# Kernel optimization log

Hardware: AMD Instinct MI355X
Metric: run time of the kernel (lower is better)

The kernel has to match this reference:

```python
import jax, jax.numpy as jnp
import numpy as np

B, T, I, H = 4096, 512, 4, 64  # batch, seq_len, input_size, hidden_size


def setup_inputs() -> dict:
    key = jax.random.key(0)
    ks = jax.random.split(key, 13)
    sc = 1.0 / np.sqrt(H)
    sc2 = 1.0 / np.sqrt(32)
    n = lambda k, shape, s: (jax.random.normal(k, shape, jnp.float32) * s)
    return {
        "x": jax.random.normal(ks[0], (B, T, I), jnp.float32),
        # PyTorch LSTM layout: gates stacked as [i, f, g, o] along first dim
        "w_ih0": n(ks[1], (4 * H, I), sc),
        "w_hh0": n(ks[2], (4 * H, H), sc),
        "b_ih0": n(ks[3], (4 * H,), sc),
        "b_hh0": n(ks[4], (4 * H,), sc),
        "w_ih1": n(ks[5], (4 * H, H), sc),
        "w_hh1": n(ks[6], (4 * H, H), sc),
        "b_ih1": n(ks[7], (4 * H,), sc),
        "b_hh1": n(ks[8], (4 * H,), sc),
        "fc1_w": n(ks[9], (32, H), sc),
        "fc1_b": n(ks[10], (32,), sc),
        "fc2_w": n(ks[11], (2, 32), sc2),
        "fc2_b": n(ks[12], (2,), sc2),
    }


def _lstm_layer(x, w_ih, w_hh, b_ih, b_hh):
    # x: [B, T, D_in] -> hidden sequence [B, T, H]
    Bq = x.shape[0]
    Hq = w_hh.shape[1]
    # Precompute input contribution for all timesteps in one GEMM
    pre = jnp.einsum('bti,gi->btg', x, w_ih) + b_ih + b_hh  # [B, T, 4H]
    pre = jnp.swapaxes(pre, 0, 1)  # [T, B, 4H] for scan

    def step(carry, xt):
        h, c = carry
        gates = xt + h @ w_hh.T  # [B, 4H]
        i, f, g, o = jnp.split(gates, 4, axis=-1)
        c_new = jax.nn.sigmoid(f) * c + jax.nn.sigmoid(i) * jnp.tanh(g)
        h_new = jax.nn.sigmoid(o) * jnp.tanh(c_new)
        return (h_new, c_new), h_new

    h0 = jnp.zeros((Bq, Hq), x.dtype)
    _, hs = jax.lax.scan(step, (h0, h0), pre)
    return jnp.swapaxes(hs, 0, 1)  # [B, T, H]


def reference(x, w_ih0, w_hh0, b_ih0, b_hh0, w_ih1, w_hh1, b_ih1, b_hh1,
              fc1_w, fc1_b, fc2_w, fc2_b):
    h1 = _lstm_layer(x, w_ih0, w_hh0, b_ih0, b_hh0)
    # dropout(p=0.2) between LSTM layers is inactive in eval mode
    h2 = _lstm_layer(h1, w_ih1, w_hh1, b_ih1, b_hh1)
    last = h2[:, -1, :]  # [B, H]
    y = jax.nn.relu(last @ fc1_w.T + fc1_b)
    return jax.nn.relu(y @ fc2_w.T + fc2_b)  # [B, 2]
```

## Files before the change

### kernel.cpp

```cpp
#include <hip/hip_runtime.h>

#define TT 512
#define MM 16

typedef _Float16 f16_t;
typedef f16_t f16x8 __attribute__((ext_vector_type(8)));
typedef float  f32x4 __attribute__((ext_vector_type(4)));
typedef unsigned uintx4 __attribute__((ext_vector_type(4)));

#define MFMA16(A, B, C) __builtin_amdgcn_mfma_f32_16x16x32_f16((A), (B), (C), 0, 0, 0)

__device__ __forceinline__ float fr(float x) { return __builtin_amdgcn_rcpf(x); }

#if __has_builtin(__builtin_amdgcn_exp2f)
__device__ __forceinline__ float ex2(float x) { return __builtin_amdgcn_exp2f(x); }
#define EXS 1.44269504f
#else
__device__ __forceinline__ float ex2(float x) { return __expf(x); }
#define EXS 1.0f
#endif

#if __has_builtin(__builtin_amdgcn_cvt_pkrtz)
__device__ __forceinline__ unsigned pk2(float a, float b) {
    auto p = __builtin_amdgcn_cvt_pkrtz(a, b);
    return __builtin_bit_cast(unsigned, p);
}
#else
__device__ __forceinline__ unsigned pk2(float a, float b) {
    unsigned short ha = __builtin_bit_cast(unsigned short, (f16_t)a);
    unsigned short hb = __builtin_bit_cast(unsigned short, (f16_t)b);
    return (unsigned)ha | ((unsigned)hb << 16);
}
#endif

__device__ __forceinline__ void bar() {
    asm volatile("s_waitcnt lgkmcnt(0)" ::: "memory");
    __builtin_amdgcn_s_barrier();
    asm volatile("" ::: "memory");
}

__device__ __forceinline__ float cellEW(float pi, float pf, float pg, float po,
                                        float4 bq, float& c) {
    float A = ex2(fmaf(pf, -EXS, bq.y));
    float B = ex2(fmaf(pi, -EXS, bq.x));
    float C = ex2(fmaf(pg, 2.f * EXS, bq.z));
    float oa = 1.f + A;
    float u  = (1.f + B) * (C + 1.f);
    float cn = fmaf(c, u, oa * (C - 1.f)) * fr(oa * u);
    c = cn;
    float D = ex2(fmaf(po, -EXS, bq.w));
    float E = ex2(fminf(2.f * EXS * cn, 30.f));
    return (E - 1.f) * fr((1.f + D) * (E + 1.f));
}

__device__ __forceinline__ f16x8 cvt8(const float* p) {
    f16x8 r;
#pragma unroll
    for (int e = 0; e < 8; ++e) r[e] = (f16_t)p[e];
    return r;
}


__global__ __launch_bounds__(512, 2) void lstm_v11(
    const float* __restrict__ x,
    const float* __restrict__ w_ih0, const float* __restrict__ w_hh0,
    const float* __restrict__ b_ih0, const float* __restrict__ b_hh0,
    const float* __restrict__ w_ih1, const float* __restrict__ w_hh1,
    const float* __restrict__ b_ih1, const float* __restrict__ b_hh1,
    const float* __restrict__ fc1_w, const float* __restrict__ fc1_b,
    const float* __restrict__ fc2_w, const float* __restrict__ fc2_b,
    float* __restrict__ out)
{
    __shared__ __align__(16) unsigned h1p[2][512];
    __shared__ __align__(16) unsigned h2p[2][512];
    __shared__ __align__(16) float sH[MM * 68];
    __shared__ float sY[MM * 34];

    const int tid = threadIdx.x;
    const int l   = tid & 63;
    const int wv  = tid >> 6;
    const int rbase = blockIdx.x * MM;

    const int lc = l & 15;
    const int lq = l >> 4;
    const bool isL1 = (wv >= 4);
    const int wsub = wv & 3;
    const int hc0  = wsub * 16 + lq * 4;
    const int swz  = (lc & 7) << 4;

    const int rdo0 = (lc * 128 + 0 * 64 + lq * 16) ^ swz;
    const int rdo1 = (lc * 128 + 1 * 64 + lq * 16) ^ swz;
    const int wro  = (lc * 128 + hc0 * 2) ^ swz;
    const unsigned xmask = (lq == 0) ? 0xFFFFFFFFu : 0u;

    f16x8 wA[4][2];
    f16x8 wB[4][2];
    f16x8 wx[4];
    float4 bq[4];
#pragma unroll
    for (int g = 0; g < 4; ++g) {
        const int grow = (g * 64 + wsub * 16 + lc) * 64 + lq * 8;
        if (isL1) {
            wA[g][0] = cvt8(w_hh0 + grow);
            wA[g][1] = cvt8(w_hh0 + grow + 32);
            const int ga = (g * 64 + wsub * 16 + lc) * 4;
#pragma unroll
            for (int e = 0; e < 8; ++e)
                wx[g][e] = (e < 4 && lq == 0) ? (f16_t)w_ih0[ga + e] : (f16_t)0.f;
        } else {
            wA[g][0] = cvt8(w_ih1 + grow);
            wA[g][1] = cvt8(w_ih1 + grow + 32);
            wB[g][0] = cvt8(w_hh1 + grow);
            wB[g][1] = cvt8(w_hh1 + grow + 32);
        }
    }
#pragma unroll
    for (int q = 0; q < 4; ++q) {
        const int hc = hc0 + q;
        float b[4];
#pragma unroll
        for (int g = 0; g < 4; ++g) {
            const int ga = g * 64 + hc;
            b[g] = isL1 ? (b_ih0[ga] + b_hh0[ga]) : (b_ih1[ga] + b_hh1[ga]);
        }
        bq[q] = make_float4(-EXS * b[0], -EXS * b[1], 2.f * EXS * b[2], -EXS * b[3]);
    }

    float c_st[4] = {0.f, 0.f, 0.f, 0.f};
    const f32x4 z4 = {0.f, 0.f, 0.f, 0.f};

    const float4* xg = (const float4*)x;
    const size_t xrow = (size_t)(rbase + lc) * TT;
    float4 xq = make_float4(0, 0, 0, 0);
    const float4* xp = xg + xrow + 2;
    if (isL1) xq = xg[xrow + 1];

    if (isL1) {
        float4 x0 = xg[xrow + 0];
        unsigned a0 = pk2(x0.x, x0.y) & xmask, a1 = pk2(x0.z, x0.w) & xmask;
        uintx4 uv = {a0, a1, 0u, 0u};
        f16x8 xf = __builtin_bit_cast(f16x8, uv);
        f32x4 a[4];
#pragma unroll
        for (int g = 0; g < 4; ++g) a[g] = MFMA16(wx[g], xf, z4);
        float hv[4];
#pragma unroll
        for (int q = 0; q < 4; ++q)
            hv[q] = cellEW(a[0][q], a[1][q], a[2][q], a[3][q], bq[q], c_st[q]);
        uint2 w2 = make_uint2(pk2(hv[0], hv[1]), pk2(hv[2], hv[3]));
        *(uint2*)((char*)h1p[0] + wro) = w2;
    } else {
        h2p[0][tid] = 0;
        h2p[0][256 + tid] = 0;
    }
    __syncthreads();

    auto STEP = [&](const unsigned* h1r, unsigned* h1w,
                    const unsigned* h2r, unsigned* h2w,
                    bool l1act, bool pref, bool lastStore) {
        if (isL1) {
            if (l1act) {
                const char* pl = (const char*)h1r;
                f16x8 hf0 = *(const f16x8*)(pl + rdo0);
                f16x8 hf1 = *(const f16x8*)(pl + rdo1);
                float4 xn;
                if (pref) { xn = *xp; ++xp; }
                unsigned a0 = pk2(xq.x, xq.y) & xmask, a1 = pk2(xq.z, xq.w) & xmask;
                uintx4 uv = {a0, a1, 0u, 0u};
                f16x8 xf = __builtin_bit_cast(f16x8, uv);

                f32x4 a[4];
                __builtin_amdgcn_s_setprio(1);
#pragma unroll
                for (int g = 0; g < 4; ++g) {
                    a[g] = MFMA16(wx[g], xf, z4);
                    a[g] = MFMA16(wA[g][0], hf0, a[g]);
                    a[g] = MFMA16(wA[g][1], hf1, a[g]);
                }
                __builtin_amdgcn_s_setprio(0);

                float hv[4];
#pragma unroll
                for (int q = 0; q < 4; ++q)
                    hv[q] = cellEW(a[0][q], a[1][q], a[2][q], a[3][q], bq[q], c_st[q]);
                uint2 w2 = make_uint2(pk2(hv[0], hv[1]), pk2(hv[2], hv[3]));
                *(uint2*)((char*)h1w + wro) = w2;
                if (pref) xq = xn;
            }
        } else {
            const char* pl1 = (const char*)h1r;
            const char* pl2 = (const char*)h2r;
            f16x8 hf0 = *(const f16x8*)(pl1 + rdo0);
            f16x8 hf1 = *(const f16x8*)(pl1 + rdo1);
            f16x8 gf0 = *(const f16x8*)(pl2 + rdo0);
            f16x8 gf1 = *(const f16x8*)(pl2 + rdo1);

            f32x4 a[4];
            __builtin_amdgcn_s_setprio(1);
#pragma unroll
            for (int g = 0; g < 4; ++g) {
                a[g] = MFMA16(wA[g][0], hf0, z4);
                a[g] = MFMA16(wA[g][1], hf1, a[g]);
                a[g] = MFMA16(wB[g][0], gf0, a[g]);
                a[g] = MFMA16(wB[g][1], gf1, a[g]);
            }
            __builtin_amdgcn_s_setprio(0);

            float hv[4];
#pragma unroll
            for (int q = 0; q < 4; ++q)
                hv[q] = cellEW(a[0][q], a[1][q], a[2][q], a[3][q], bq[q], c_st[q]);
            uint2 w2 = make_uint2(pk2(hv[0], hv[1]), pk2(hv[2], hv[3]));
            *(uint2*)((char*)h2w + wro) = w2;
            if (lastStore)
                *(float4*)&sH[lc * 68 + hc0] = make_float4(hv[0], hv[1], hv[2], hv[3]);
        }
        bar();
    };

    for (int it = 0; it < 255; ++it) {
        STEP(h1p[0], h1p[1], h2p[0], h2p[1], true, true, false);
        STEP(h1p[1], h1p[0], h2p[1], h2p[0], true, true, false);
    }
    STEP(h1p[0], h1p[1], h2p[0], h2p[1], true, false, false);
    STEP(h1p[1], h1p[0], h2p[1], h2p[0], false, false, true);

    {
        const int r = tid >> 5, mo = tid & 31;
        float s = fc1_b[mo];
#pragma unroll 8
        for (int k = 0; k < 64; ++k) s = fmaf(sH[r * 68 + k], fc1_w[mo * 64 + k], s);
        sY[r * 34 + mo] = fmaxf(s, 0.f);
    }
    __syncthreads();
    if (tid < 32) {
        const int r = tid >> 1, o = tid & 1;
        float s = fc2_b[o];
#pragma unroll 8
        for (int mo = 0; mo < 32; ++mo) s = fmaf(sY[r * 34 + mo], fc2_w[o * 32 + mo], s);
        out[(size_t)(rbase + r) * 2 + o] = fmaxf(s, 0.f);
    }
}

extern "C" void kernel_launch(void* const* d_in, const int* in_sizes, int n_in,
                              void* d_out, int out_size, void* d_ws, size_t ws_size,
                              hipStream_t stream) {
    const float* x     = (const float*)d_in[0];
    const float* w_ih0 = (const float*)d_in[1];
    const float* w_hh0 = (const float*)d_in[2];
    const float* b_ih0 = (const float*)d_in[3];
    const float* b_hh0 = (const float*)d_in[4];
    const float* w_ih1 = (const float*)d_in[5];
    const float* w_hh1 = (const float*)d_in[6];
    const float* b_ih1 = (const float*)d_in[7];
    const float* b_hh1 = (const float*)d_in[8];
    const float* fc1_w = (const float*)d_in[9];
    const float* fc1_b = (const float*)d_in[10];
    const float* fc2_w = (const float*)d_in[11];
    const float* fc2_b = (const float*)d_in[12];
    float* out = (float*)d_out;

    const int nB   = in_sizes[0] / (TT * 4);
    const int grid = nB / MM;

    lstm_v11<<<grid, 512, 0, stream>>>(x, w_ih0, w_hh0, b_ih0, b_hh0,
                                       w_ih1, w_hh1, b_ih1, b_hh1,
                                       fc1_w, fc1_b, fc2_w, fc2_b, out);
}
```

Measured before the change: 370.2 us.

## Split each LSTM step into two phases so MFMA and elementwise overlap across layers

Each timestep now runs in two barrier-separated phases. Layer-1 waves do their MFMAs while layer-2 waves do the elementwise cell update for the previous step, and then the roles swap. Layer-2 gate accumulators are carried across phases in registers, and its hidden state drops to a single shared buffer. The goal is to keep the matrix unit and vector ALU busy at the same time instead of running each wave's MFMA and transcendental work back to back. In exchange there are twice as many block barriers per timestep and extra live registers, which could hurt occupancy at 512 threads with 2 blocks.

```diff
diff --git a/kernel.cpp b/kernel.cpp
--- a/kernel.cpp
+++ b/kernel.cpp
@@ -61,7 +61,7 @@
 }
 
 
-__global__ __launch_bounds__(512, 2) void lstm_v11(
+__global__ __launch_bounds__(512, 2) void lstm_v12(
     const float* __restrict__ x,
     const float* __restrict__ w_ih0, const float* __restrict__ w_hh0,
     const float* __restrict__ b_ih0, const float* __restrict__ b_hh0,
@@ -72,7 +72,7 @@
     float* __restrict__ out)
 {
     __shared__ __align__(16) unsigned h1p[2][512];
-    __shared__ __align__(16) unsigned h2p[2][512];
+    __shared__ __align__(16) unsigned h2p[512];
     __shared__ __align__(16) float sH[MM * 68];
     __shared__ float sY[MM * 34];
 
@@ -128,6 +128,7 @@
 
     float c_st[4] = {0.f, 0.f, 0.f, 0.f};
     const f32x4 z4 = {0.f, 0.f, 0.f, 0.f};
+    f32x4 a2s[4];
 
     const float4* xg = (const float4*)x;
     const size_t xrow = (size_t)(rbase + lc) * TT;
@@ -137,8 +138,8 @@
 
     if (isL1) {
         float4 x0 = xg[xrow + 0];
-        unsigned a0 = pk2(x0.x, x0.y) & xmask, a1 = pk2(x0.z, x0.w) & xmask;
-        uintx4 uv = {a0, a1, 0u, 0u};
+        unsigned u0 = pk2(x0.x, x0.y) & xmask, u1 = pk2(x0.z, x0.w) & xmask;
+        uintx4 uv = {u0, u1, 0u, 0u};
         f16x8 xf = __builtin_bit_cast(f16x8, uv);
         f32x4 a[4];
 #pragma unroll
@@ -150,14 +151,14 @@
         uint2 w2 = make_uint2(pk2(hv[0], hv[1]), pk2(hv[2], hv[3]));
         *(uint2*)((char*)h1p[0] + wro) = w2;
     } else {
-        h2p[0][tid] = 0;
-        h2p[0][256 + tid] = 0;
+        h2p[tid] = 0;
+        h2p[256 + tid] = 0;
     }
     __syncthreads();
 
     auto STEP = [&](const unsigned* h1r, unsigned* h1w,
-                    const unsigned* h2r, unsigned* h2w,
-                    bool l1act, bool pref, bool lastStore) {
+                    bool l1act, bool pref, bool ew2act) {
+        f32x4 a1[4];
         if (isL1) {
             if (l1act) {
                 const char* pl = (const char*)h1r;
@@ -165,65 +166,76 @@
                 f16x8 hf1 = *(const f16x8*)(pl + rdo1);
                 float4 xn;
                 if (pref) { xn = *xp; ++xp; }
-                unsigned a0 = pk2(xq.x, xq.y) & xmask, a1 = pk2(xq.z, xq.w) & xmask;
-                uintx4 uv = {a0, a1, 0u, 0u};
+                unsigned u0 = pk2(xq.x, xq.y) & xmask, u1 = pk2(xq.z, xq.w) & xmask;
+                uintx4 uv = {u0, u1, 0u, 0u};
                 f16x8 xf = __builtin_bit_cast(f16x8, uv);
-
-                f32x4 a[4];
                 __builtin_amdgcn_s_setprio(1);
 #pragma unroll
                 for (int g = 0; g < 4; ++g) {
-                    a[g] = MFMA16(wx[g], xf, z4);
-                    a[g] = MFMA16(wA[g][0], hf0, a[g]);
-                    a[g] = MFMA16(wA[g][1], hf1, a[g]);
+                    a1[g] = MFMA16(wx[g], xf, z4);
+                    a1[g] = MFMA16(wA[g][0], hf0, a1[g]);
+                    a1[g] = MFMA16(wA[g][1], hf1, a1[g]);
                 }
                 __builtin_amdgcn_s_setprio(0);
-
+                if (pref) xq = xn;
+            }
+        } else {
+            if (ew2act) {
                 float hv[4];
 #pragma unroll
                 for (int q = 0; q < 4; ++q)
-                    hv[q] = cellEW(a[0][q], a[1][q], a[2][q], a[3][q], bq[q], c_st[q]);
+                    hv[q] = cellEW(a2s[0][q], a2s[1][q], a2s[2][q], a2s[3][q], bq[q], c_st[q]);
+                uint2 w2 = make_uint2(pk2(hv[0], hv[1]), pk2(hv[2], hv[3]));
+                *(uint2*)((char*)h2p + wro) = w2;
+            }
+        }
+        bar();
+        if (isL1) {
+            if (l1act) {
+                float hv[4];
+#pragma unroll
+                for (int q = 0; q < 4; ++q)
+                    hv[q] = cellEW(a1[0][q], a1[1][q], a1[2][q], a1[3][q], bq[q], c_st[q]);
                 uint2 w2 = make_uint2(pk2(hv[0], hv[1]), pk2(hv[2], hv[3]));
                 *(uint2*)((char*)h1w + wro) = w2;
-                if (pref) xq = xn;
             }
         } else {
             const char* pl1 = (const char*)h1r;
-            const char* pl2 = (const char*)h2r;
+            const char* pl2 = (const char*)h2p;
             f16x8 hf0 = *(const f16x8*)(pl1 + rdo0);
             f16x8 hf1 = *(const f16x8*)(pl1 + rdo1);
             f16x8 gf0 = *(const f16x8*)(pl2 + rdo0);
             f16x8 gf1 = *(const f16x8*)(pl2 + rdo1);
-
-            f32x4 a[4];
             __builtin_amdgcn_s_setprio(1);
 #pragma unroll
             for (int g = 0; g < 4; ++g) {
-                a[g] = MFMA16(wA[g][0], hf0, z4);
-                a[g] = MFMA16(wA[g][1], hf1, a[g]);
-                a[g] = MFMA16(wB[g][0], gf0, a[g]);
-                a[g] = MFMA16(wB[g][1], gf1, a[g]);
+                a2s[g] = MFMA16(wA[g][0], hf0, z4);
+                a2s[g] = MFMA16(wA[g][1], hf1, a2s[g]);
+                a2s[g] = MFMA16(wB[g][0], gf0, a2s[g]);
+                a2s[g] = MFMA16(wB[g][1], gf1, a2s[g]);
             }
             __builtin_amdgcn_s_setprio(0);
-
-            float hv[4];
-#pragma unroll
-            for (int q = 0; q < 4; ++q)
-                hv[q] = cellEW(a[0][q], a[1][q], a[2][q], a[3][q], bq[q], c_st[q]);
-            uint2 w2 = make_uint2(pk2(hv[0], hv[1]), pk2(hv[2], hv[3]));
-            *(uint2*)((char*)h2w + wro) = w2;
-            if (lastStore)
-                *(float4*)&sH[lc * 68 + hc0] = make_float4(hv[0], hv[1], hv[2], hv[3]);
         }
         bar();
     };
 
-    for (int it = 0; it < 255; ++it) {
-        STEP(h1p[0], h1p[1], h2p[0], h2p[1], true, true, false);
-        STEP(h1p[1], h1p[0], h2p[1], h2p[0], true, true, false);
-    }
-    STEP(h1p[0], h1p[1], h2p[0], h2p[1], true, false, false);
-    STEP(h1p[1], h1p[0], h2p[1], h2p[0], false, false, true);
+    STEP(h1p[0], h1p[1], true, true, false);
+    for (int k = 0; k < 254; ++k) {
+        STEP(h1p[1], h1p[0], true, true, true);
+        STEP(h1p[0], h1p[1], true, true, true);
+    }
+    STEP(h1p[1], h1p[0], true, true,  true);
+    STEP(h1p[0], h1p[1], true, false, true);
+    STEP(h1p[1], h1p[0], false, false, true);
+
+    if (!isL1) {
+        float hv[4];
+#pragma unroll
+        for (int q = 0; q < 4; ++q)
+            hv[q] = cellEW(a2s[0][q], a2s[1][q], a2s[2][q], a2s[3][q], bq[q], c_st[q]);
+        *(float4*)&sH[lc * 68 + hc0] = make_float4(hv[0], hv[1], hv[2], hv[3]);
+    }
+    __syncthreads();
 
     {
         const int r = tid >> 5, mo = tid & 31;
@@ -263,7 +275,7 @@
     const int nB   = in_sizes[0] / (TT * 4);
     const int grid = nB / MM;
 
-    lstm_v11<<<grid, 512, 0, stream>>>(x, w_ih0, w_hh0, b_ih0, b_hh0,
+    lstm_v12<<<grid, 512, 0, stream>>>(x, w_ih0, w_hh0, b_ih0, b_hh0,
                                        w_ih1, w_hh1, b_ih1, b_hh1,
                                        fc1_w, fc1_b, fc2_w, fc2_b, out);
 }
```

Measured after the change: 436.1 us. 1.18x slower.

## Stage packed fp16 input sequence in LDS up front; raise layer-2 wave priority

Applied to the files above, without the earlier changes.

Before the recurrence, the block loads the full 16-row x 512-step input tile, packs it to fp16 and stores it in 64KB of dynamic shared memory. Each layer-1 step then reads its x fragment from LDS instead of issuing a global load on the serial critical path. Lanes that previously masked x to zero now read from a small zero buffer. The per-step setprio toggles are replaced by a persistent high priority for the layer-2 waves. LDS use rises to about 80KB per block, which at two blocks per CU may limit occupancy, and there is an upfront load phase before any compute starts.

```diff
diff --git a/kernel.cpp b/kernel.cpp
--- a/kernel.cpp
+++ b/kernel.cpp
@@ -61,7 +61,9 @@
 }
 
 
-__global__ __launch_bounds__(512, 2) void lstm_v11(
+#define SMEM_BYTES 80272
+
+__global__ __launch_bounds__(512, 2) void lstm_v14(
     const float* __restrict__ x,
     const float* __restrict__ w_ih0, const float* __restrict__ w_hh0,
     const float* __restrict__ b_ih0, const float* __restrict__ b_hh0,
@@ -71,10 +73,13 @@
     const float* __restrict__ fc2_w, const float* __restrict__ fc2_b,
     float* __restrict__ out)
 {
-    __shared__ __align__(16) unsigned h1p[2][512];
-    __shared__ __align__(16) unsigned h2p[2][512];
-    __shared__ __align__(16) float sH[MM * 68];
-    __shared__ float sY[MM * 34];
+    extern __shared__ __align__(16) char sm[];
+    unsigned* xpk = (unsigned*)(sm);
+    unsigned (*h1p)[512] = (unsigned(*)[512])(sm + 65536);
+    unsigned (*h2p)[512] = (unsigned(*)[512])(sm + 69632);
+    unsigned* zq = (unsigned*)(sm + 73728);
+    float* sH = (float*)(sm + 73744);
+    float* sY = (float*)(sm + 78096);
 
     const int tid = threadIdx.x;
     const int l   = tid & 63;
@@ -91,7 +96,21 @@
     const int rdo0 = (lc * 128 + 0 * 64 + lq * 16) ^ swz;
     const int rdo1 = (lc * 128 + 1 * 64 + lq * 16) ^ swz;
     const int wro  = (lc * 128 + hc0 * 2) ^ swz;
-    const unsigned xmask = (lq == 0) ? 0xFFFFFFFFu : 0u;
+
+    {
+        const float4* xsrc = (const float4*)x;
+        for (int j = tid; j < 16 * 512; j += 512) {
+            const int row = j >> 9;
+            const int tt  = j & 511;
+            float4 v = xsrc[(size_t)(rbase + row) * TT + tt];
+            uint2 w = make_uint2(pk2(v.x, v.y), pk2(v.z, v.w));
+            *(uint2*)((char*)xpk + (size_t)(tt * 16 + row) * 8) = w;
+        }
+        if (tid == 0) { zq[0] = 0; zq[1] = 0; zq[2] = 0; zq[3] = 0; }
+    }
+    const char* xbp  = (lq == 0) ? ((const char*)xpk + (16 + lc) * 8) : (const char*)zq;
+    const char* x0p  = (lq == 0) ? ((const char*)xpk + lc * 8)        : (const char*)zq;
+    const int   xstr = (lq == 0) ? 128 : 0;
 
     f16x8 wA[4][2];
     f16x8 wB[4][2];
@@ -129,16 +148,11 @@
     float c_st[4] = {0.f, 0.f, 0.f, 0.f};
     const f32x4 z4 = {0.f, 0.f, 0.f, 0.f};
 
-    const float4* xg = (const float4*)x;
-    const size_t xrow = (size_t)(rbase + lc) * TT;
-    float4 xq = make_float4(0, 0, 0, 0);
-    const float4* xp = xg + xrow + 2;
-    if (isL1) xq = xg[xrow + 1];
+    __syncthreads();
 
     if (isL1) {
-        float4 x0 = xg[xrow + 0];
-        unsigned a0 = pk2(x0.x, x0.y) & xmask, a1 = pk2(x0.z, x0.w) & xmask;
-        uintx4 uv = {a0, a1, 0u, 0u};
+        uint2 x0 = *(const uint2*)x0p;
+        uintx4 uv = {x0.x, x0.y, 0u, 0u};
         f16x8 xf = __builtin_bit_cast(f16x8, uv);
         f32x4 a[4];
 #pragma unroll
@@ -154,6 +168,8 @@
         h2p[0][256 + tid] = 0;
     }
     __syncthreads();
+
+    if (!isL1) __builtin_amdgcn_s_setprio(1);
 
     auto STEP = [&](const unsigned* h1r, unsigned* h1w,
                     const unsigned* h2r, unsigned* h2w,
@@ -163,29 +179,24 @@
                 const char* pl = (const char*)h1r;
                 f16x8 hf0 = *(const f16x8*)(pl + rdo0);
                 f16x8 hf1 = *(const f16x8*)(pl + rdo1);
-                float4 xn;
-                if (pref) { xn = *xp; ++xp; }
-                unsigned a0 = pk2(xq.x, xq.y) & xmask, a1 = pk2(xq.z, xq.w) & xmask;
-                uintx4 uv = {a0, a1, 0u, 0u};
+                uint2 xu = *(const uint2*)xbp;
+                if (pref) xbp += xstr;
+                uintx4 uv = {xu.x, xu.y, 0u, 0u};
                 f16x8 xf = __builtin_bit_cast(f16x8, uv);
 
                 f32x4 a[4];
-                __builtin_amdgcn_s_setprio(1);
 #pragma unroll
                 for (int g = 0; g < 4; ++g) {
                     a[g] = MFMA16(wx[g], xf, z4);
                     a[g] = MFMA16(wA[g][0], hf0, a[g]);
                     a[g] = MFMA16(wA[g][1], hf1, a[g]);
                 }
-                __builtin_amdgcn_s_setprio(0);
-
                 float hv[4];
 #pragma unroll
                 for (int q = 0; q < 4; ++q)
                     hv[q] = cellEW(a[0][q], a[1][q], a[2][q], a[3][q], bq[q], c_st[q]);
                 uint2 w2 = make_uint2(pk2(hv[0], hv[1]), pk2(hv[2], hv[3]));
                 *(uint2*)((char*)h1w + wro) = w2;
-                if (pref) xq = xn;
             }
         } else {
             const char* pl1 = (const char*)h1r;
@@ -196,7 +207,6 @@
             f16x8 gf1 = *(const f16x8*)(pl2 + rdo1);
 
             f32x4 a[4];
-            __builtin_amdgcn_s_setprio(1);
 #pragma unroll
             for (int g = 0; g < 4; ++g) {
                 a[g] = MFMA16(wA[g][0], hf0, z4);
@@ -204,8 +214,6 @@
                 a[g] = MFMA16(wB[g][0], gf0, a[g]);
                 a[g] = MFMA16(wB[g][1], gf1, a[g]);
             }
-            __builtin_amdgcn_s_setprio(0);
-
             float hv[4];
 #pragma unroll
             for (int q = 0; q < 4; ++q)
@@ -224,6 +232,8 @@
     }
     STEP(h1p[0], h1p[1], h2p[0], h2p[1], true, false, false);
     STEP(h1p[1], h1p[0], h2p[1], h2p[0], false, false, true);
+
+    if (!isL1) __builtin_amdgcn_s_setprio(0);
 
     {
         const int r = tid >> 5, mo = tid & 31;
@@ -263,7 +273,10 @@
     const int nB   = in_sizes[0] / (TT * 4);
     const int grid = nB / MM;
 
-    lstm_v11<<<grid, 512, 0, stream>>>(x, w_ih0, w_hh0, b_ih0, b_hh0,
-                                       w_ih1, w_hh1, b_ih1, b_hh1,
-                                       fc1_w, fc1_b, fc2_w, fc2_b, out);
-}
+    hipFuncSetAttribute(reinterpret_cast<const void*>(lstm_v14),
+                        hipFuncAttributeMaxDynamicSharedMemorySize, SMEM_BYTES);
+
+    lstm_v14<<<grid, 512, SMEM_BYTES, stream>>>(x, w_ih0, w_hh0, b_ih0, b_hh0,
+                                                w_ih1, w_hh1, b_ih1, b_hh1,
+                                                fc1_w, fc1_b, fc2_w, fc2_b, out);
+}
```

Result: no change. 371.3 us (+0.3%).

## Merge both LSTM layers into each wave, halving block size to four waves

Applied to the files above, without the earlier changes.

Instead of dedicating four waves to layer 1 and four to layer 2, each of four waves now holds weights for both layers and computes both layer recurrences every step. Layer-2 MFMAs are issued first and layer-1 MFMAs are interleaved with the layer-2 cell nonlinearities to overlap matrix and vector work. This reduces the number of waves participating in each barrier but doubles per-wave register pressure and serial work per step, lowering available wave-level parallelism per CU.

```diff
diff --git a/kernel.cpp b/kernel.cpp
--- a/kernel.cpp
+++ b/kernel.cpp
@@ -61,7 +61,7 @@
 }
 
 
-__global__ __launch_bounds__(512, 2) void lstm_v11(
+__global__ __launch_bounds__(256, 1) void lstm_v15(
     const float* __restrict__ x,
     const float* __restrict__ w_ih0, const float* __restrict__ w_hh0,
     const float* __restrict__ b_ih0, const float* __restrict__ b_hh0,
@@ -83,9 +83,7 @@
 
     const int lc = l & 15;
     const int lq = l >> 4;
-    const bool isL1 = (wv >= 4);
-    const int wsub = wv & 3;
-    const int hc0  = wsub * 16 + lq * 4;
+    const int hc0  = wv * 16 + lq * 4;
     const int swz  = (lc & 7) << 4;
 
     const int rdo0 = (lc * 128 + 0 * 64 + lq * 16) ^ swz;
@@ -93,52 +91,52 @@
     const int wro  = (lc * 128 + hc0 * 2) ^ swz;
     const unsigned xmask = (lq == 0) ? 0xFFFFFFFFu : 0u;
 
-    f16x8 wA[4][2];
-    f16x8 wB[4][2];
+    f16x8 w1A[4][2];
     f16x8 wx[4];
-    float4 bq[4];
+    f16x8 w2A[4][2];
+    f16x8 w2B[4][2];
+    float4 bq1[4], bq2[4];
 #pragma unroll
     for (int g = 0; g < 4; ++g) {
-        const int grow = (g * 64 + wsub * 16 + lc) * 64 + lq * 8;
-        if (isL1) {
-            wA[g][0] = cvt8(w_hh0 + grow);
-            wA[g][1] = cvt8(w_hh0 + grow + 32);
-            const int ga = (g * 64 + wsub * 16 + lc) * 4;
-#pragma unroll
-            for (int e = 0; e < 8; ++e)
-                wx[g][e] = (e < 4 && lq == 0) ? (f16_t)w_ih0[ga + e] : (f16_t)0.f;
-        } else {
-            wA[g][0] = cvt8(w_ih1 + grow);
-            wA[g][1] = cvt8(w_ih1 + grow + 32);
-            wB[g][0] = cvt8(w_hh1 + grow);
-            wB[g][1] = cvt8(w_hh1 + grow + 32);
-        }
+        const int grow = (g * 64 + wv * 16 + lc) * 64 + lq * 8;
+        w1A[g][0] = cvt8(w_hh0 + grow);
+        w1A[g][1] = cvt8(w_hh0 + grow + 32);
+        w2A[g][0] = cvt8(w_ih1 + grow);
+        w2A[g][1] = cvt8(w_ih1 + grow + 32);
+        w2B[g][0] = cvt8(w_hh1 + grow);
+        w2B[g][1] = cvt8(w_hh1 + grow + 32);
+        const int ga = (g * 64 + wv * 16 + lc) * 4;
+#pragma unroll
+        for (int e = 0; e < 8; ++e)
+            wx[g][e] = (e < 4 && lq == 0) ? (f16_t)w_ih0[ga + e] : (f16_t)0.f;
     }
 #pragma unroll
     for (int q = 0; q < 4; ++q) {
         const int hc = hc0 + q;
-        float b[4];
+        float b1[4], b2[4];
 #pragma unroll
         for (int g = 0; g < 4; ++g) {
             const int ga = g * 64 + hc;
-            b[g] = isL1 ? (b_ih0[ga] + b_hh0[ga]) : (b_ih1[ga] + b_hh1[ga]);
+            b1[g] = b_ih0[ga] + b_hh0[ga];
+            b2[g] = b_ih1[ga] + b_hh1[ga];
         }
-        bq[q] = make_float4(-EXS * b[0], -EXS * b[1], 2.f * EXS * b[2], -EXS * b[3]);
-    }
-
-    float c_st[4] = {0.f, 0.f, 0.f, 0.f};
+        bq1[q] = make_float4(-EXS * b1[0], -EXS * b1[1], 2.f * EXS * b1[2], -EXS * b1[3]);
+        bq2[q] = make_float4(-EXS * b2[0], -EXS * b2[1], 2.f * EXS * b2[2], -EXS * b2[3]);
+    }
+
+    float c1[4] = {0.f, 0.f, 0.f, 0.f};
+    float c2[4] = {0.f, 0.f, 0.f, 0.f};
     const f32x4 z4 = {0.f, 0.f, 0.f, 0.f};
 
     const float4* xg = (const float4*)x;
     const size_t xrow = (size_t)(rbase + lc) * TT;
-    float4 xq = make_float4(0, 0, 0, 0);
     const float4* xp = xg + xrow + 2;
-    if (isL1) xq = xg[xrow + 1];
-
-    if (isL1) {
+    float4 xq = xg[xrow + 1];
+
+    {
         float4 x0 = xg[xrow + 0];
-        unsigned a0 = pk2(x0.x, x0.y) & xmask, a1 = pk2(x0.z, x0.w) & xmask;
-        uintx4 uv = {a0, a1, 0u, 0u};
+        unsigned u0 = pk2(x0.x, x0.y) & xmask, u1 = pk2(x0.z, x0.w) & xmask;
+        uintx4 uv = {u0, u1, 0u, 0u};
         f16x8 xf = __builtin_bit_cast(f16x8, uv);
         f32x4 a[4];
 #pragma unroll
@@ -146,10 +144,9 @@
         float hv[4];
 #pragma unroll
         for (int q = 0; q < 4; ++q)
-            hv[q] = cellEW(a[0][q], a[1][q], a[2][q], a[3][q], bq[q], c_st[q]);
+            hv[q] = cellEW(a[0][q], a[1][q], a[2][q], a[3][q], bq1[q], c1[q]);
         uint2 w2 = make_uint2(pk2(hv[0], hv[1]), pk2(hv[2], hv[3]));
         *(uint2*)((char*)h1p[0] + wro) = w2;
-    } else {
         h2p[0][tid] = 0;
         h2p[0][256 + tid] = 0;
     }
@@ -158,63 +155,57 @@
     auto STEP = [&](const unsigned* h1r, unsigned* h1w,
                     const unsigned* h2r, unsigned* h2w,
                     bool l1act, bool pref, bool lastStore) {
-        if (isL1) {
-            if (l1act) {
-                const char* pl = (const char*)h1r;
-                f16x8 hf0 = *(const f16x8*)(pl + rdo0);
-                f16x8 hf1 = *(const f16x8*)(pl + rdo1);
-                float4 xn;
-                if (pref) { xn = *xp; ++xp; }
-                unsigned a0 = pk2(xq.x, xq.y) & xmask, a1 = pk2(xq.z, xq.w) & xmask;
-                uintx4 uv = {a0, a1, 0u, 0u};
-                f16x8 xf = __builtin_bit_cast(f16x8, uv);
-
-                f32x4 a[4];
-                __builtin_amdgcn_s_setprio(1);
-#pragma unroll
-                for (int g = 0; g < 4; ++g) {
-                    a[g] = MFMA16(wx[g], xf, z4);
-                    a[g] = MFMA16(wA[g][0], hf0, a[g]);
-                    a[g] = MFMA16(wA[g][1], hf1, a[g]);
-                }
-                __builtin_amdgcn_s_setprio(0);
-
-                float hv[4];
-#pragma unroll
-                for (int q = 0; q < 4; ++q)
-                    hv[q] = cellEW(a[0][q], a[1][q], a[2][q], a[3][q], bq[q], c_st[q]);
-                uint2 w2 = make_uint2(pk2(hv[0], hv[1]), pk2(hv[2], hv[3]));
-                *(uint2*)((char*)h1w + wro) = w2;
-                if (pref) xq = xn;
+        const char* pl1 = (const char*)h1r;
+        const char* pl2 = (const char*)h2r;
+        f16x8 hf0 = *(const f16x8*)(pl1 + rdo0);
+        f16x8 hf1 = *(const f16x8*)(pl1 + rdo1);
+        f16x8 gf0 = *(const f16x8*)(pl2 + rdo0);
+        f16x8 gf1 = *(const f16x8*)(pl2 + rdo1);
+
+        f32x4 a2[4];
+#pragma unroll
+        for (int g = 0; g < 4; ++g) {
+            a2[g] = MFMA16(w2A[g][0], hf0, z4);
+            a2[g] = MFMA16(w2A[g][1], hf1, a2[g]);
+            a2[g] = MFMA16(w2B[g][0], gf0, a2[g]);
+            a2[g] = MFMA16(w2B[g][1], gf1, a2[g]);
+        }
+
+        float hv2[4];
+        if (l1act) {
+            float4 xn;
+            if (pref) { xn = *xp; ++xp; }
+            unsigned u0 = pk2(xq.x, xq.y) & xmask, u1 = pk2(xq.z, xq.w) & xmask;
+            uintx4 uv = {u0, u1, 0u, 0u};
+            f16x8 xf = __builtin_bit_cast(f16x8, uv);
+
+            f32x4 a1[4];
+#pragma unroll
+            for (int j = 0; j < 4; ++j) {
+                a1[j] = MFMA16(wx[j], xf, z4);
+                a1[j] = MFMA16(w1A[j][0], hf0, a1[j]);
+                a1[j] = MFMA16(w1A[j][1], hf1, a1[j]);
+                hv2[j] = cellEW(a2[0][j], a2[1][j], a2[2][j], a2[3][j], bq2[j], c2[j]);
             }
+            uint2 wh2 = make_uint2(pk2(hv2[0], hv2[1]), pk2(hv2[2], hv2[3]));
+            *(uint2*)((char*)h2w + wro) = wh2;
+
+            float hv1[4];
+#pragma unroll
+            for (int q = 0; q < 4; ++q)
+                hv1[q] = cellEW(a1[0][q], a1[1][q], a1[2][q], a1[3][q], bq1[q], c1[q]);
+            uint2 wh1 = make_uint2(pk2(hv1[0], hv1[1]), pk2(hv1[2], hv1[3]));
+            *(uint2*)((char*)h1w + wro) = wh1;
+            if (pref) xq = xn;
         } else {
-            const char* pl1 = (const char*)h1r;
-            const char* pl2 = (const char*)h2r;
-            f16x8 hf0 = *(const f16x8*)(pl1 + rdo0);
-            f16x8 hf1 = *(const f16x8*)(pl1 + rdo1);
-            f16x8 gf0 = *(const f16x8*)(pl2 + rdo0);
-            f16x8 gf1 = *(const f16x8*)(pl2 + rdo1);
-
-            f32x4 a[4];
-            __builtin_amdgcn_s_setprio(1);
-#pragma unroll
-            for (int g = 0; g < 4; ++g) {
-                a[g] = MFMA16(wA[g][0], hf0, z4);
-                a[g] = MFMA16(wA[g][1], hf1, a[g]);
-                a[g] = MFMA16(wB[g][0], gf0, a[g]);
-                a[g] = MFMA16(wB[g][1], gf1, a[g]);
-            }
-            __builtin_amdgcn_s_setprio(0);
-
-            float hv[4];
-#pragma unroll
-            for (int q = 0; q < 4; ++q)
-                hv[q] = cellEW(a[0][q], a[1][q], a[2][q], a[3][q], bq[q], c_st[q]);
-            uint2 w2 = make_uint2(pk2(hv[0], hv[1]), pk2(hv[2], hv[3]));
-            *(uint2*)((char*)h2w + wro) = w2;
-            if (lastStore)
-                *(float4*)&sH[lc * 68 + hc0] = make_float4(hv[0], hv[1], hv[2], hv[3]);
+#pragma unroll
+            for (int j = 0; j < 4; ++j)
+                hv2[j] = cellEW(a2[0][j], a2[1][j], a2[2][j], a2[3][j], bq2[j], c2[j]);
+            uint2 wh2 = make_uint2(pk2(hv2[0], hv2[1]), pk2(hv2[2], hv2[3]));
+            *(uint2*)((char*)h2w + wro) = wh2;
         }
+        if (lastStore)
+            *(float4*)&sH[lc * 68 + hc0] = make_float4(hv2[0], hv2[1], hv2[2], hv2[3]);
         bar();
     };
 
@@ -225,8 +216,8 @@
     STEP(h1p[0], h1p[1], h2p[0], h2p[1], true, false, false);
     STEP(h1p[1], h1p[0], h2p[1], h2p[0], false, false, true);
 
-    {
-        const int r = tid >> 5, mo = tid & 31;
+    for (int idx = tid; idx < MM * 32; idx += 256) {
+        const int r = idx >> 5, mo = idx & 31;
         float s = fc1_b[mo];
 #pragma unroll 8
         for (int k = 0; k < 64; ++k) s = fmaf(sH[r * 68 + k], fc1_w[mo * 64 + k], s);
@@ -263,7 +254,7 @@
     const int nB   = in_sizes[0] / (TT * 4);
     const int grid = nB / MM;
 
-    lstm_v11<<<grid, 512, 0, stream>>>(x, w_ih0, w_hh0, b_ih0, b_hh0,
+    lstm_v15<<<grid, 256, 0, stream>>>(x, w_ih0, w_hh0, b_ih0, b_hh0,
                                        w_ih1, w_hh1, b_ih1, b_hh1,
                                        fc1_w, fc1_b, fc2_w, fc2_b, out);
 }
```

Result: slower. 414.8 us (+12.0%).
